# Performance work log

Measured on AMD Instinct MI355X. Metric: run time of the kernel, lower is better.

The kernel has to match this reference:

```python
import jax, jax.numpy as jnp
import numpy as np

N, E, F_IN, H, C = 20000, 320000, 256, 4, 64
D = H * C  # hidden_dim = 256
NEG_SLOPE = 0.2
LN_EPS = 1e-5


def setup_inputs() -> dict:
    key = jax.random.key(0)
    ks = jax.random.split(key, 12)
    x = jax.random.normal(ks[0], (N, F_IN), dtype=jnp.float32)
    # edges guaranteed self-loop-free (PyG GATConv removes then re-adds self loops)
    dst = jax.random.randint(ks[1], (E,), 0, N)
    off = jax.random.randint(ks[2], (E,), 1, N)
    src = (dst + off) % N
    edge_index = jnp.stack([src, dst]).astype(jnp.int64)

    def lin(k, fan_in, shape):
        return jax.random.normal(k, shape, dtype=jnp.float32) / np.sqrt(fan_in)

    W1 = lin(ks[3], F_IN, (F_IN, D)); b1 = jnp.zeros((D,), jnp.float32)
    a_src1 = lin(ks[4], C, (H, C)); a_dst1 = lin(ks[5], C, (H, C))
    W2 = lin(ks[6], D, (D, D)); b2 = jnp.zeros((D,), jnp.float32)
    a_src2 = lin(ks[7], C, (H, C)); a_dst2 = lin(ks[8], C, (H, C))
    g1 = jnp.ones((D,), jnp.float32); be1 = jnp.zeros((D,), jnp.float32)
    g2 = jnp.ones((D,), jnp.float32); be2 = jnp.zeros((D,), jnp.float32)
    attn_w = lin(ks[9], D, (D, 1)); attn_b = jnp.zeros((1,), jnp.float32)
    return dict(x=x, edge_index=edge_index, W1=W1, b1=b1, a_src1=a_src1,
                a_dst1=a_dst1, W2=W2, b2=b2, a_src2=a_src2, a_dst2=a_dst2,
                g1=g1, be1=be1, g2=g2, be2=be2, attn_w=attn_w, attn_b=attn_b)


def _gat_conv(x, src, dst, W, b, a_src, a_dst):
    # x: [N, F] -> h: [N, H, C]
    h = (x @ W).reshape(N, H, C)
    alpha_s = jnp.einsum('nhc,hc->nh', h, a_src)  # [N, H]
    alpha_d = jnp.einsum('nhc,hc->nh', h, a_dst)
    e = jax.nn.leaky_relu(alpha_s[src] + alpha_d[dst], NEG_SLOPE)  # [E', H]
    # segment softmax over edges sharing a destination
    m = jax.ops.segment_max(e, dst, num_segments=N)
    w = jnp.exp(e - m[dst])
    z = jax.ops.segment_sum(w, dst, num_segments=N)
    alpha = w / (z[dst] + 1e-16)
    out = jax.ops.segment_sum(h[src] * alpha[:, :, None], dst, num_segments=N)
    return out.reshape(N, D) + b


def _layernorm(x, g, b):
    mu = x.mean(-1, keepdims=True)
    var = ((x - mu) ** 2).mean(-1, keepdims=True)
    return (x - mu) * jax.lax.rsqrt(var + LN_EPS) * g + b


def reference(x, edge_index, W1, b1, a_src1, a_dst1, W2, b2, a_src2, a_dst2,
              g1, be1, g2, be2, attn_w, attn_b):
    loops = jnp.arange(N, dtype=edge_index.dtype)
    src = jnp.concatenate([edge_index[0], loops])
    dst = jnp.concatenate([edge_index[1], loops])
    x1 = _gat_conv(x, src, dst, W1, b1, a_src1, a_dst1)
    x1 = jax.nn.elu(_layernorm(x1, g1, be1))
    x2 = _gat_conv(x1, src, dst, W2, b2, a_src2, a_dst2)
    x2 = jax.nn.elu(_layernorm(x2, g2, be2) + x1)
    attn = jax.nn.softmax(x2 @ attn_w + attn_b, axis=0)  # softmax over nodes
    pooled = (x2 * attn).sum(axis=0)  # [D]
    return pooled
```

## Files before the change

### kernel.cpp

```cpp
#include <hip/hip_runtime.h>
#include <math.h>

#define N_NODES 20000
#define E_EDGES 320000
#define TOT_E   (E_EDGES + N_NODES)
#define DHID    256
#define NHEAD   4
#define SCAN_NB ((N_NODES + 255) / 256)

typedef float f32x4 __attribute__((ext_vector_type(4)));
typedef short short8 __attribute__((ext_vector_type(8)));
typedef unsigned short ushort;

__device__ __forceinline__ float wave_sum(float v) {
#pragma unroll
  for (int off = 32; off; off >>= 1) v += __shfl_xor(v, off);
  return v;
}
__device__ __forceinline__ ushort f2bf(float f) {
  unsigned u = __float_as_uint(f);
  u += 0x7fffu + ((u >> 16) & 1u);
  return (ushort)(u >> 16);
}
__device__ __forceinline__ float bflo(unsigned u) {
  return __uint_as_float(u << 16);
}
__device__ __forceinline__ float bfhi(unsigned u) {
  return __uint_as_float(u & 0xffff0000u);
}

__global__ void hist_kernel(const int* __restrict__ ei, int* __restrict__ deg) {
  int e = blockIdx.x * blockDim.x + threadIdx.x;
  if (e >= TOT_E) return;
  int dst = (e < E_EDGES) ? ei[E_EDGES + e] : (e - E_EDGES);
  atomicAdd(&deg[dst], 1);
}

__global__ __launch_bounds__(256)
void scan_blocks_kernel(const int* __restrict__ deg, int* __restrict__ bsum) {
  __shared__ int ws[4];
  const int t = threadIdx.x;
  const int i = blockIdx.x * 256 + t;
  int v = (i < N_NODES) ? deg[i] : 0;
  int s = v;
#pragma unroll
  for (int off = 32; off; off >>= 1) s += __shfl_xor(s, off);
  if ((t & 63) == 0) ws[t >> 6] = s;
  __syncthreads();
  if (t == 0) bsum[blockIdx.x] = ws[0] + ws[1] + ws[2] + ws[3];
}

__global__ __launch_bounds__(128)
void scan_tops_kernel(const int* __restrict__ bsum, int* __restrict__ boff) {
  __shared__ int tmp[SCAN_NB];
  const int t = threadIdx.x;
  if (t < SCAN_NB) tmp[t] = bsum[t];
  __syncthreads();
  if (t == 0) {
    int run = 0;
    for (int i = 0; i < SCAN_NB; ++i) { int x = tmp[i]; tmp[i] = run; run += x; }
  }
  __syncthreads();
  if (t < SCAN_NB) boff[t] = tmp[t];
}

__global__ __launch_bounds__(256)
void scan_apply_kernel(const int* __restrict__ deg, const int* __restrict__ boff,
                       int* __restrict__ rowp, int* __restrict__ cur) {
  __shared__ int ws[4];
  const int t = threadIdx.x;
  const int lane = t & 63, w = t >> 6;
  const int i = blockIdx.x * 256 + t;
  int v = (i < N_NODES) ? deg[i] : 0;
  int inc = v;
#pragma unroll
  for (int off = 1; off < 64; off <<= 1) {
    int u = __shfl_up(inc, off);
    if (lane >= off) inc += u;
  }
  if (lane == 63) ws[w] = inc;
  __syncthreads();
  int add = boff[blockIdx.x];
#pragma unroll
  for (int k = 0; k < 4; ++k)
    if (k < w) add += ws[k];
  int exc = add + inc - v;
  if (i < N_NODES) {
    rowp[i] = exc;
    cur[i] = exc;
    if (i == N_NODES - 1) rowp[N_NODES] = exc + v;
  }
}

__global__ void scatter_kernel(const int* __restrict__ ei, int* __restrict__ cur,
                               int* __restrict__ colb) {
  int e = blockIdx.x * blockDim.x + threadIdx.x;
  if (e >= TOT_E) return;
  int src, dst;
  if (e < E_EDGES) { src = ei[e]; dst = ei[E_EDGES + e]; }
  else             { src = dst = e - E_EDGES; }
  int pos = atomicAdd(&cur[dst], 1);
  colb[pos] = src;
}

__global__ __launch_bounds__(256)
void conv_inputs_kernel(const float* __restrict__ W1, const float* __restrict__ W2,
                        const float* __restrict__ x, ushort* __restrict__ Wt1,
                        ushort* __restrict__ Wt2, ushort* __restrict__ xb) {
  const int b = blockIdx.x;
  if (b < 512) {
    const float* W = (b < 256) ? W1 : W2;
    ushort* Wt = (b < 256) ? Wt1 : Wt2;
    const int n = b & 255;
    const int k = threadIdx.x;
    Wt[n * 256 + k] = f2bf(W[k * 256 + n]);
  } else {
    int idx = (b - 512) * 256 + threadIdx.x;
    size_t base = (size_t)idx * 8;
    float4 a = *reinterpret_cast<const float4*>(x + base);
    float4 c = *reinterpret_cast<const float4*>(x + base + 4);
    short8 o;
    o[0] = f2bf(a.x); o[1] = f2bf(a.y); o[2] = f2bf(a.z); o[3] = f2bf(a.w);
    o[4] = f2bf(c.x); o[5] = f2bf(c.y); o[6] = f2bf(c.z); o[7] = f2bf(c.w);
    *reinterpret_cast<short8*>(xb + base) = o;
  }
}

__global__ __launch_bounds__(256)
void gemm_alpha_kernel(const ushort* __restrict__ Ab, const ushort* __restrict__ Wt,
                       const float* __restrict__ asrc, const float* __restrict__ adst,
                       ushort* __restrict__ hout, float* __restrict__ as_,
                       float* __restrict__ ad_) {
  __shared__ ushort hs[32 * 256];

  const int t = threadIdx.x;
  const int w = t >> 6;
  const int l = t & 63;
  const int row0 = blockIdx.x * 32;

  const ushort* abase = Ab + (size_t)(row0 + (l & 15)) * 256 + ((l >> 4) * 8);
  const ushort* bbase = Wt + (size_t)(w * 64 + (l & 15)) * 256 + ((l >> 4) * 8);

  f32x4 acc[2][4];
#pragma unroll
  for (int i = 0; i < 2; ++i)
#pragma unroll
    for (int j = 0; j < 4; ++j) acc[i][j] = (f32x4){0.f, 0.f, 0.f, 0.f};

  short8 a0 = *reinterpret_cast<const short8*>(abase);
  short8 a1 = *reinterpret_cast<const short8*>(abase + 16 * 256);
  short8 b0 = *reinterpret_cast<const short8*>(bbase);
  short8 b1 = *reinterpret_cast<const short8*>(bbase + 16 * 256);
  short8 b2 = *reinterpret_cast<const short8*>(bbase + 32 * 256);
  short8 b3 = *reinterpret_cast<const short8*>(bbase + 48 * 256);
#pragma unroll
  for (int kk = 0; kk < 256; kk += 32) {
    short8 na0, na1, nb0, nb1, nb2, nb3;
    if (kk + 32 < 256) {
      na0 = *reinterpret_cast<const short8*>(abase + kk + 32);
      na1 = *reinterpret_cast<const short8*>(abase + 16 * 256 + kk + 32);
      nb0 = *reinterpret_cast<const short8*>(bbase + kk + 32);
      nb1 = *reinterpret_cast<const short8*>(bbase + 16 * 256 + kk + 32);
      nb2 = *reinterpret_cast<const short8*>(bbase + 32 * 256 + kk + 32);
      nb3 = *reinterpret_cast<const short8*>(bbase + 48 * 256 + kk + 32);
    }
    acc[0][0] = __builtin_amdgcn_mfma_f32_16x16x32_bf16(a0, b0, acc[0][0], 0, 0, 0);
    acc[0][1] = __builtin_amdgcn_mfma_f32_16x16x32_bf16(a0, b1, acc[0][1], 0, 0, 0);
    acc[0][2] = __builtin_amdgcn_mfma_f32_16x16x32_bf16(a0, b2, acc[0][2], 0, 0, 0);
    acc[0][3] = __builtin_amdgcn_mfma_f32_16x16x32_bf16(a0, b3, acc[0][3], 0, 0, 0);
    acc[1][0] = __builtin_amdgcn_mfma_f32_16x16x32_bf16(a1, b0, acc[1][0], 0, 0, 0);
    acc[1][1] = __builtin_amdgcn_mfma_f32_16x16x32_bf16(a1, b1, acc[1][1], 0, 0, 0);
    acc[1][2] = __builtin_amdgcn_mfma_f32_16x16x32_bf16(a1, b2, acc[1][2], 0, 0, 0);
    acc[1][3] = __builtin_amdgcn_mfma_f32_16x16x32_bf16(a1, b3, acc[1][3], 0, 0, 0);
    if (kk + 32 < 256) {
      a0 = na0; a1 = na1; b0 = nb0; b1 = nb1; b2 = nb2; b3 = nb3;
    }
  }

  float asj[4], adj[4];
#pragma unroll
  for (int j = 0; j < 4; ++j) {
    asj[j] = asrc[w * 64 + j * 16 + (l & 15)];
    adj[j] = adst[w * 64 + j * 16 + (l & 15)];
  }
#pragma unroll
  for (int i = 0; i < 2; ++i) {
#pragma unroll
    for (int q = 0; q < 4; ++q) {
      float ps = 0.f, pd = 0.f;
#pragma unroll
      for (int j = 0; j < 4; ++j) {
        ps += acc[i][j][q] * asj[j];
        pd += acc[i][j][q] * adj[j];
      }
#pragma unroll
      for (int off = 1; off < 16; off <<= 1) {
        ps += __shfl_xor(ps, off);
        pd += __shfl_xor(pd, off);
      }
      int row = row0 + i * 16 + (l >> 4) * 4 + q;
      if ((l & 15) == 0) {
        as_[row * 4 + w] = ps;
        ad_[row * 4 + w] = pd;
      }
    }
  }

#pragma unroll
  for (int i = 0; i < 2; ++i)
#pragma unroll
    for (int j = 0; j < 4; ++j)
#pragma unroll
      for (int q = 0; q < 4; ++q) {
        int row = i * 16 + (l >> 4) * 4 + q;
        int col = w * 64 + j * 16 + (l & 15);
        hs[row * 256 + col] = f2bf(acc[i][j][q]);
      }
  __syncthreads();
#pragma unroll
  for (int g = 0; g < 4; ++g) {
    int gi = g * 256 + t;
    int row = gi >> 5;
    int slot = gi & 31;
    *reinterpret_cast<short8*>(hout + (size_t)(row0 + row) * 256 + slot * 8) =
        *reinterpret_cast<const short8*>(&hs[row * 256 + slot * 8]);
  }
}

__global__ __launch_bounds__(256)
void attn_w_kernel(const float* __restrict__ as_, const float* __restrict__ ad_,
                   const int* __restrict__ rowp, const int* __restrict__ colb,
                   float* __restrict__ wbuf, float* __restrict__ zinv) {
  const int t = threadIdx.x;
  const int d = blockIdx.x * 4 + (t >> 6);
  const int l = t & 63;
  const int e16 = l >> 2;
  const int hh = l & 3;
  const int start = rowp[d];
  const int deg = rowp[d + 1] - start;
  const float adv = ad_[d * 4 + hh];

  float M = -INFINITY;
  for (int base = 0; base < deg; base += 16) {
    int i = base + e16;
    float ev = -INFINITY;
    if (i < deg) {
      int s = colb[start + i];
      float e = as_[s * 4 + hh] + adv;
      ev = (e >= 0.f) ? e : 0.2f * e;
    }
    M = fmaxf(M, ev);
  }
#pragma unroll
  for (int off = 4; off < 64; off <<= 1) M = fmaxf(M, __shfl_xor(M, off));

  float z = 0.f;
  for (int base = 0; base < deg; base += 16) {
    int i = base + e16;
    if (i < deg) {
      int s = colb[start + i];
      float e = as_[s * 4 + hh] + adv;
      e = (e >= 0.f) ? e : 0.2f * e;
      float wv = __expf(e - M);
      wbuf[(size_t)(start + i) * 4 + hh] = wv;
      z += wv;
    }
  }
#pragma unroll
  for (int off = 4; off < 64; off <<= 1) z += __shfl_xor(z, off);
  if (e16 == 0) zinv[d * 4 + hh] = 1.f / (z + 1e-16f);
}

__global__ __launch_bounds__(256)
void gather_ln_kernel(const ushort* __restrict__ h, const int* __restrict__ rowp,
                      const int* __restrict__ colb, const float* __restrict__ wbuf,
                      const float* __restrict__ zinv, const float* __restrict__ bias,
                      const float* __restrict__ gamma, const float* __restrict__ beta,
                      const ushort* __restrict__ residb, float* __restrict__ outf,
                      ushort* __restrict__ outb, const float* __restrict__ aw,
                      const float* __restrict__ ab, float* __restrict__ score) {
  const int t = threadIdx.x;
  const int d = blockIdx.x * 4 + (t >> 6);
  const int l = t & 63;
  const int hh = l >> 4;
  const int c0 = l * 4;
  const int start = rowp[d];
  const int deg = rowp[d + 1] - start;

  float a0 = 0.f, a1 = 0.f, a2 = 0.f, a3 = 0.f;
  const ushort* hrow = h + c0;
#pragma unroll 2
  for (int i = 0; i < deg; ++i) {
    const int slot = start + i;
    int s = colb[slot];
    float wv = wbuf[(size_t)slot * 4 + hh];
    uint2 hv = *reinterpret_cast<const uint2*>(hrow + (size_t)s * 256);
    a0 += wv * bflo(hv.x);
    a1 += wv * bfhi(hv.x);
    a2 += wv * bflo(hv.y);
    a3 += wv * bfhi(hv.y);
  }
  const float zi = zinv[d * 4 + hh];
  float4 bi = *reinterpret_cast<const float4*>(bias + c0);
  float v0 = a0 * zi + bi.x, v1 = a1 * zi + bi.y;
  float v2 = a2 * zi + bi.z, v3 = a3 * zi + bi.w;

  float s1 = wave_sum(v0 + v1 + v2 + v3);
  float s2 = wave_sum(v0 * v0 + v1 * v1 + v2 * v2 + v3 * v3);
  float mu = s1 * (1.f / 256.f);
  float var = s2 * (1.f / 256.f) - mu * mu;
  float rstd = rsqrtf(var + 1e-5f);
  float4 ga = *reinterpret_cast<const float4*>(gamma + c0);
  float4 be = *reinterpret_cast<const float4*>(beta + c0);
  float y0 = (v0 - mu) * rstd * ga.x + be.x;
  float y1 = (v1 - mu) * rstd * ga.y + be.y;
  float y2 = (v2 - mu) * rstd * ga.z + be.z;
  float y3 = (v3 - mu) * rstd * ga.w + be.w;
  if (residb) {
    uint2 rv = *reinterpret_cast<const uint2*>(residb + (size_t)d * 256 + c0);
    y0 += bflo(rv.x); y1 += bfhi(rv.x); y2 += bflo(rv.y); y3 += bfhi(rv.y);
  }
  y0 = (y0 > 0.f) ? y0 : expm1f(y0);
  y1 = (y1 > 0.f) ? y1 : expm1f(y1);
  y2 = (y2 > 0.f) ? y2 : expm1f(y2);
  y3 = (y3 > 0.f) ? y3 : expm1f(y3);

  if (outb) {
    uint2 o;
    o.x = ((unsigned)f2bf(y0)) | (((unsigned)f2bf(y1)) << 16);
    o.y = ((unsigned)f2bf(y2)) | (((unsigned)f2bf(y3)) << 16);
    *reinterpret_cast<uint2*>(outb + (size_t)d * 256 + c0) = o;
  }
  if (outf) {
    *reinterpret_cast<float4*>(outf + (size_t)d * 256 + c0) =
        make_float4(y0, y1, y2, y3);
  }
  if (score) {
    float4 aww = *reinterpret_cast<const float4*>(aw + c0);
    float sp = wave_sum(y0 * aww.x + y1 * aww.y + y2 * aww.z + y3 * aww.w);
    if (l == 0) score[d] = sp + ab[0];
  }
}

__global__ __launch_bounds__(256)
void softmax_reduce_kernel(const float* __restrict__ s, float* __restrict__ mz) {
  __shared__ float red[4];
  const int t = threadIdx.x, lane = t & 63, wid = t >> 6;
  float m = -INFINITY;
  for (int n4 = t; n4 < N_NODES / 4; n4 += 256) {
    float4 v = *reinterpret_cast<const float4*>(s + n4 * 4);
    m = fmaxf(m, fmaxf(fmaxf(v.x, v.y), fmaxf(v.z, v.w)));
  }
#pragma unroll
  for (int off = 32; off; off >>= 1) m = fmaxf(m, __shfl_xor(m, off));
  if (lane == 0) red[wid] = m;
  __syncthreads();
  m = fmaxf(fmaxf(red[0], red[1]), fmaxf(red[2], red[3]));
  __syncthreads();
  float z = 0.f;
  for (int n4 = t; n4 < N_NODES / 4; n4 += 256) {
    float4 v = *reinterpret_cast<const float4*>(s + n4 * 4);
    z += __expf(v.x - m) + __expf(v.y - m) + __expf(v.z - m) + __expf(v.w - m);
  }
  z = wave_sum(z);
  if (lane == 0) red[wid] = z;
  __syncthreads();
  if (t == 0) { mz[0] = m; mz[1] = red[0] + red[1] + red[2] + red[3]; }
}

__global__ __launch_bounds__(256)
void pool_partial_kernel(const float* __restrict__ x2, const float* __restrict__ s,
                         const float* __restrict__ mz, float* __restrict__ part) {
  __shared__ float red4[4][256];
  const int t = threadIdx.x, b = blockIdx.x;
  const int c4 = t & 63, rsub = t >> 6;
  const float m = mz[0];
  const float invz = 1.f / mz[1];
  f32x4 acc = (f32x4){0.f, 0.f, 0.f, 0.f};
  for (int n = b * 4 + rsub; n < N_NODES; n += 1024) {
    float w = __expf(s[n] - m);
    float4 xv = *reinterpret_cast<const float4*>(&x2[(size_t)n * 256 + c4 * 4]);
    acc[0] += w * xv.x; acc[1] += w * xv.y; acc[2] += w * xv.z; acc[3] += w * xv.w;
  }
#pragma unroll
  for (int k = 0; k < 4; ++k) red4[rsub][c4 * 4 + k] = acc[k];
  __syncthreads();
  if (t < 256) {
    float v = red4[0][t] + red4[1][t] + red4[2][t] + red4[3][t];
    part[b * 256 + t] = v * invz;
  }
}

__global__ __launch_bounds__(256)
void pool_final_kernel(const float* __restrict__ part, float* __restrict__ out) {
  const int t = threadIdx.x;
  float acc = 0.f;
  for (int b = 0; b < 256; ++b) acc += part[b * 256 + t];
  out[t] = acc;
}

extern "C" void kernel_launch(void* const* d_in, const int* in_sizes, int n_in,
                              void* d_out, int out_size, void* d_ws, size_t ws_size,
                              hipStream_t stream) {
  const float* x      = (const float*)d_in[0];
  const int*   ei     = (const int*)d_in[1];
  const float* W1     = (const float*)d_in[2];
  const float* b1     = (const float*)d_in[3];
  const float* a_src1 = (const float*)d_in[4];
  const float* a_dst1 = (const float*)d_in[5];
  const float* W2     = (const float*)d_in[6];
  const float* b2     = (const float*)d_in[7];
  const float* a_src2 = (const float*)d_in[8];
  const float* a_dst2 = (const float*)d_in[9];
  const float* g1     = (const float*)d_in[10];
  const float* be1    = (const float*)d_in[11];
  const float* g2     = (const float*)d_in[12];
  const float* be2    = (const float*)d_in[13];
  const float* attn_w = (const float*)d_in[14];
  const float* attn_b = (const float*)d_in[15];
  float* out = (float*)d_out;

  char* p = (char*)d_ws;
  auto alloc = [&](size_t bytes) {
    char* r = p;
    p += (bytes + 255) & ~size_t(255);
    return r;
  };
  ushort* h   = (ushort*)alloc((size_t)N_NODES * 256 * 2);
  ushort* xb  = (ushort*)alloc((size_t)N_NODES * 256 * 2);
  ushort* xb1 = (ushort*)alloc((size_t)N_NODES * 256 * 2);
  float* x2   = (float*)alloc((size_t)N_NODES * 256 * 4);
  float* as_  = (float*)alloc((size_t)N_NODES * 4 * 4);
  float* ad_  = (float*)alloc((size_t)N_NODES * 4 * 4);
  float* zinv = (float*)alloc((size_t)N_NODES * 4 * 4);
  float* wbuf = (float*)alloc((size_t)TOT_E * 4 * 4);
  float* sbuf = (float*)alloc((size_t)N_NODES * 4);
  float* mz   = (float*)alloc(256);
  float* part = (float*)alloc((size_t)256 * 256 * 4);
  ushort* wt1 = (ushort*)alloc((size_t)256 * 256 * 2);
  ushort* wt2 = (ushort*)alloc((size_t)256 * 256 * 2);
  int* deg    = (int*)alloc((size_t)N_NODES * 4);
  int* rowp   = (int*)alloc((size_t)(N_NODES + 1) * 4);
  int* cur    = (int*)alloc((size_t)N_NODES * 4);
  int* colb   = (int*)alloc((size_t)TOT_E * 4);
  int* bsum   = (int*)alloc((size_t)SCAN_NB * 4);
  int* boff   = (int*)alloc((size_t)SCAN_NB * 4);

  const int EB = (TOT_E + 255) / 256;
  const int GB = N_NODES / 32;
  const int DB = N_NODES / 4;

  hipMemsetAsync(deg, 0, (size_t)N_NODES * 4, stream);
  hist_kernel<<<EB, 256, 0, stream>>>(ei, deg);
  conv_inputs_kernel<<<512 + N_NODES * 256 / 8 / 256, 256, 0, stream>>>(
      W1, W2, x, wt1, wt2, xb);
  scan_blocks_kernel<<<SCAN_NB, 256, 0, stream>>>(deg, bsum);
  scan_tops_kernel<<<1, 128, 0, stream>>>(bsum, boff);
  scan_apply_kernel<<<SCAN_NB, 256, 0, stream>>>(deg, boff, rowp, cur);
  scatter_kernel<<<EB, 256, 0, stream>>>(ei, cur, colb);

  gemm_alpha_kernel<<<GB, 256, 0, stream>>>(xb, wt1, a_src1, a_dst1, h, as_, ad_);
  attn_w_kernel<<<DB, 256, 0, stream>>>(as_, ad_, rowp, colb, wbuf, zinv);
  gather_ln_kernel<<<DB, 256, 0, stream>>>(h, rowp, colb, wbuf, zinv, b1, g1, be1,
                                           nullptr, nullptr, xb1,
                                           nullptr, nullptr, nullptr);
  gemm_alpha_kernel<<<GB, 256, 0, stream>>>(xb1, wt2, a_src2, a_dst2, h, as_, ad_);
  attn_w_kernel<<<DB, 256, 0, stream>>>(as_, ad_, rowp, colb, wbuf, zinv);
  gather_ln_kernel<<<DB, 256, 0, stream>>>(h, rowp, colb, wbuf, zinv, b2, g2, be2,
                                           xb1, x2, nullptr,
                                           attn_w, attn_b, sbuf);
  softmax_reduce_kernel<<<1, 256, 0, stream>>>(sbuf, mz);
  pool_partial_kernel<<<256, 256, 0, stream>>>(x2, sbuf, mz, part);
  pool_final_kernel<<<1, 256, 0, stream>>>(part, out);
}
```

Baseline: 214.6 us.

## Fuse attention weights into gather-LN kernel, store x2 as bf16, parallelize score softmax

Merges the attention-weight kernel into the gather/LayerNorm kernel. The max is still computed per destination, but exp weights and their sum are recomputed inside the feature gather loop. This removes the wbuf/zinv write and re-read round trip and one launch per layer. The final layer output is stored in bf16 instead of fp32, which halves pooling reads at some precision cost. The single-block score softmax reduction is split into 32 partial blocks plus a combine kernel, and the deg memset is folded into the conversion kernel. The trade-off is an extra as_ gather and exp per edge for every lane of the gather loop.

```diff
diff --git a/kernel.cpp b/kernel.cpp
--- a/kernel.cpp
+++ b/kernel.cpp
@@ -7,6 +7,7 @@
 #define DHID    256
 #define NHEAD   4
 #define SCAN_NB ((N_NODES + 255) / 256)
+#define SPART   32
 
 typedef float f32x4 __attribute__((ext_vector_type(4)));
 typedef short short8 __attribute__((ext_vector_type(8)));
@@ -106,7 +107,8 @@
 __global__ __launch_bounds__(256)
 void conv_inputs_kernel(const float* __restrict__ W1, const float* __restrict__ W2,
                         const float* __restrict__ x, ushort* __restrict__ Wt1,
-                        ushort* __restrict__ Wt2, ushort* __restrict__ xb) {
+                        ushort* __restrict__ Wt2, ushort* __restrict__ xb,
+                        int* __restrict__ deg) {
   const int b = blockIdx.x;
   if (b < 512) {
     const float* W = (b < 256) ? W1 : W2;
@@ -114,7 +116,7 @@
     const int n = b & 255;
     const int k = threadIdx.x;
     Wt[n * 256 + k] = f2bf(W[k * 256 + n]);
-  } else {
+  } else if (b < 512 + N_NODES * 256 / 8 / 256) {
     int idx = (b - 512) * 256 + threadIdx.x;
     size_t base = (size_t)idx * 8;
     float4 a = *reinterpret_cast<const float4*>(x + base);
@@ -123,6 +125,9 @@
     o[0] = f2bf(a.x); o[1] = f2bf(a.y); o[2] = f2bf(a.z); o[3] = f2bf(a.w);
     o[4] = f2bf(c.x); o[5] = f2bf(c.y); o[6] = f2bf(c.z); o[7] = f2bf(c.w);
     *reinterpret_cast<short8*>(xb + base) = o;
+  } else {
+    int idx = (b - (512 + N_NODES * 256 / 8 / 256)) * 256 + threadIdx.x;
+    if (idx < N_NODES) deg[idx] = 0;
   }
 }
 
@@ -228,79 +233,52 @@
 }
 
 __global__ __launch_bounds__(256)
-void attn_w_kernel(const float* __restrict__ as_, const float* __restrict__ ad_,
-                   const int* __restrict__ rowp, const int* __restrict__ colb,
-                   float* __restrict__ wbuf, float* __restrict__ zinv) {
+void attn_gather_ln_kernel(const ushort* __restrict__ h, const float* __restrict__ as_,
+                           const float* __restrict__ ad_, const int* __restrict__ rowp,
+                           const int* __restrict__ colb, const float* __restrict__ bias,
+                           const float* __restrict__ gamma, const float* __restrict__ beta,
+                           const ushort* __restrict__ residb, ushort* __restrict__ outb,
+                           const float* __restrict__ aw, const float* __restrict__ ab,
+                           float* __restrict__ score) {
   const int t = threadIdx.x;
   const int d = blockIdx.x * 4 + (t >> 6);
   const int l = t & 63;
-  const int e16 = l >> 2;
-  const int hh = l & 3;
   const int start = rowp[d];
   const int deg = rowp[d + 1] - start;
+
+  const int e16 = l >> 2, hh = l & 3;
   const float adv = ad_[d * 4 + hh];
-
   float M = -INFINITY;
-  for (int base = 0; base < deg; base += 16) {
-    int i = base + e16;
-    float ev = -INFINITY;
-    if (i < deg) {
-      int s = colb[start + i];
-      float e = as_[s * 4 + hh] + adv;
-      ev = (e >= 0.f) ? e : 0.2f * e;
-    }
-    M = fmaxf(M, ev);
+  for (int i = e16; i < deg; i += 16) {
+    int s = colb[start + i];
+    float e = as_[s * 4 + hh] + adv;
+    e = (e >= 0.f) ? e : 0.2f * e;
+    M = fmaxf(M, e);
   }
 #pragma unroll
   for (int off = 4; off < 64; off <<= 1) M = fmaxf(M, __shfl_xor(M, off));
 
-  float z = 0.f;
-  for (int base = 0; base < deg; base += 16) {
-    int i = base + e16;
-    if (i < deg) {
-      int s = colb[start + i];
-      float e = as_[s * 4 + hh] + adv;
-      e = (e >= 0.f) ? e : 0.2f * e;
-      float wv = __expf(e - M);
-      wbuf[(size_t)(start + i) * 4 + hh] = wv;
-      z += wv;
-    }
-  }
-#pragma unroll
-  for (int off = 4; off < 64; off <<= 1) z += __shfl_xor(z, off);
-  if (e16 == 0) zinv[d * 4 + hh] = 1.f / (z + 1e-16f);
-}
-
-__global__ __launch_bounds__(256)
-void gather_ln_kernel(const ushort* __restrict__ h, const int* __restrict__ rowp,
-                      const int* __restrict__ colb, const float* __restrict__ wbuf,
-                      const float* __restrict__ zinv, const float* __restrict__ bias,
-                      const float* __restrict__ gamma, const float* __restrict__ beta,
-                      const ushort* __restrict__ residb, float* __restrict__ outf,
-                      ushort* __restrict__ outb, const float* __restrict__ aw,
-                      const float* __restrict__ ab, float* __restrict__ score) {
-  const int t = threadIdx.x;
-  const int d = blockIdx.x * 4 + (t >> 6);
-  const int l = t & 63;
-  const int hh = l >> 4;
+  const int gh = l >> 4;
+  const float Mg = __shfl(M, gh);
+  const float adg = __shfl(adv, gh);
+
+  float a0 = 0.f, a1 = 0.f, a2 = 0.f, a3 = 0.f, z = 0.f;
   const int c0 = l * 4;
-  const int start = rowp[d];
-  const int deg = rowp[d + 1] - start;
-
-  float a0 = 0.f, a1 = 0.f, a2 = 0.f, a3 = 0.f;
   const ushort* hrow = h + c0;
 #pragma unroll 2
   for (int i = 0; i < deg; ++i) {
-    const int slot = start + i;
-    int s = colb[slot];
-    float wv = wbuf[(size_t)slot * 4 + hh];
+    int s = colb[start + i];
+    float e = as_[s * 4 + gh] + adg;
+    e = (e >= 0.f) ? e : 0.2f * e;
+    float wv = __expf(e - Mg);
+    z += wv;
     uint2 hv = *reinterpret_cast<const uint2*>(hrow + (size_t)s * 256);
     a0 += wv * bflo(hv.x);
     a1 += wv * bfhi(hv.x);
     a2 += wv * bflo(hv.y);
     a3 += wv * bfhi(hv.y);
   }
-  const float zi = zinv[d * 4 + hh];
+  const float zi = 1.f / (z + 1e-16f);
   float4 bi = *reinterpret_cast<const float4*>(bias + c0);
   float v0 = a0 * zi + bi.x, v1 = a1 * zi + bi.y;
   float v2 = a2 * zi + bi.z, v3 = a3 * zi + bi.w;
@@ -325,16 +303,11 @@
   y2 = (y2 > 0.f) ? y2 : expm1f(y2);
   y3 = (y3 > 0.f) ? y3 : expm1f(y3);
 
-  if (outb) {
-    uint2 o;
-    o.x = ((unsigned)f2bf(y0)) | (((unsigned)f2bf(y1)) << 16);
-    o.y = ((unsigned)f2bf(y2)) | (((unsigned)f2bf(y3)) << 16);
-    *reinterpret_cast<uint2*>(outb + (size_t)d * 256 + c0) = o;
-  }
-  if (outf) {
-    *reinterpret_cast<float4*>(outf + (size_t)d * 256 + c0) =
-        make_float4(y0, y1, y2, y3);
-  }
+  uint2 o;
+  o.x = ((unsigned)f2bf(y0)) | (((unsigned)f2bf(y1)) << 16);
+  o.y = ((unsigned)f2bf(y2)) | (((unsigned)f2bf(y3)) << 16);
+  *reinterpret_cast<uint2*>(outb + (size_t)d * 256 + c0) = o;
+
   if (score) {
     float4 aww = *reinterpret_cast<const float4*>(aw + c0);
     float sp = wave_sum(y0 * aww.x + y1 * aww.y + y2 * aww.z + y3 * aww.w);
@@ -343,14 +316,13 @@
 }
 
 __global__ __launch_bounds__(256)
-void softmax_reduce_kernel(const float* __restrict__ s, float* __restrict__ mz) {
+void score_part_kernel(const float* __restrict__ s, float* __restrict__ pm,
+                       float* __restrict__ pz) {
   __shared__ float red[4];
-  const int t = threadIdx.x, lane = t & 63, wid = t >> 6;
+  const int t = threadIdx.x, b = blockIdx.x;
+  const int lane = t & 63, wid = t >> 6;
   float m = -INFINITY;
-  for (int n4 = t; n4 < N_NODES / 4; n4 += 256) {
-    float4 v = *reinterpret_cast<const float4*>(s + n4 * 4);
-    m = fmaxf(m, fmaxf(fmaxf(v.x, v.y), fmaxf(v.z, v.w)));
-  }
+  for (int n = b * 256 + t; n < N_NODES; n += SPART * 256) m = fmaxf(m, s[n]);
 #pragma unroll
   for (int off = 32; off; off >>= 1) m = fmaxf(m, __shfl_xor(m, off));
   if (lane == 0) red[wid] = m;
@@ -358,18 +330,27 @@
   m = fmaxf(fmaxf(red[0], red[1]), fmaxf(red[2], red[3]));
   __syncthreads();
   float z = 0.f;
-  for (int n4 = t; n4 < N_NODES / 4; n4 += 256) {
-    float4 v = *reinterpret_cast<const float4*>(s + n4 * 4);
-    z += __expf(v.x - m) + __expf(v.y - m) + __expf(v.z - m) + __expf(v.w - m);
-  }
+  for (int n = b * 256 + t; n < N_NODES; n += SPART * 256) z += __expf(s[n] - m);
   z = wave_sum(z);
   if (lane == 0) red[wid] = z;
   __syncthreads();
-  if (t == 0) { mz[0] = m; mz[1] = red[0] + red[1] + red[2] + red[3]; }
-}
-
-__global__ __launch_bounds__(256)
-void pool_partial_kernel(const float* __restrict__ x2, const float* __restrict__ s,
+  if (t == 0) { pm[b] = m; pz[b] = red[0] + red[1] + red[2] + red[3]; }
+}
+
+__global__ __launch_bounds__(64)
+void score_comb_kernel(const float* __restrict__ pm, const float* __restrict__ pz,
+                       float* __restrict__ mz) {
+  const int l = threadIdx.x;
+  float m = (l < SPART) ? pm[l] : -INFINITY;
+#pragma unroll
+  for (int off = 32; off; off >>= 1) m = fmaxf(m, __shfl_xor(m, off));
+  float z = (l < SPART) ? pz[l] * __expf(pm[l] - m) : 0.f;
+  z = wave_sum(z);
+  if (l == 0) { mz[0] = m; mz[1] = z; }
+}
+
+__global__ __launch_bounds__(256)
+void pool_partial_kernel(const ushort* __restrict__ hb2, const float* __restrict__ s,
                          const float* __restrict__ mz, float* __restrict__ part) {
   __shared__ float red4[4][256];
   const int t = threadIdx.x, b = blockIdx.x;
@@ -379,8 +360,11 @@
   f32x4 acc = (f32x4){0.f, 0.f, 0.f, 0.f};
   for (int n = b * 4 + rsub; n < N_NODES; n += 1024) {
     float w = __expf(s[n] - m);
-    float4 xv = *reinterpret_cast<const float4*>(&x2[(size_t)n * 256 + c4 * 4]);
-    acc[0] += w * xv.x; acc[1] += w * xv.y; acc[2] += w * xv.z; acc[3] += w * xv.w;
+    uint2 hv = *reinterpret_cast<const uint2*>(hb2 + (size_t)n * 256 + c4 * 4);
+    acc[0] += w * bflo(hv.x);
+    acc[1] += w * bfhi(hv.x);
+    acc[2] += w * bflo(hv.y);
+    acc[3] += w * bfhi(hv.y);
   }
 #pragma unroll
   for (int k = 0; k < 4; ++k) red4[rsub][c4 * 4 + k] = acc[k];
@@ -429,13 +413,13 @@
   ushort* h   = (ushort*)alloc((size_t)N_NODES * 256 * 2);
   ushort* xb  = (ushort*)alloc((size_t)N_NODES * 256 * 2);
   ushort* xb1 = (ushort*)alloc((size_t)N_NODES * 256 * 2);
-  float* x2   = (float*)alloc((size_t)N_NODES * 256 * 4);
+  ushort* hb2 = (ushort*)alloc((size_t)N_NODES * 256 * 2);
   float* as_  = (float*)alloc((size_t)N_NODES * 4 * 4);
   float* ad_  = (float*)alloc((size_t)N_NODES * 4 * 4);
-  float* zinv = (float*)alloc((size_t)N_NODES * 4 * 4);
-  float* wbuf = (float*)alloc((size_t)TOT_E * 4 * 4);
   float* sbuf = (float*)alloc((size_t)N_NODES * 4);
   float* mz   = (float*)alloc(256);
+  float* pm   = (float*)alloc((size_t)SPART * 4);
+  float* pz   = (float*)alloc((size_t)SPART * 4);
   float* part = (float*)alloc((size_t)256 * 256 * 4);
   ushort* wt1 = (ushort*)alloc((size_t)256 * 256 * 2);
   ushort* wt2 = (ushort*)alloc((size_t)256 * 256 * 2);
@@ -449,27 +433,24 @@
   const int EB = (TOT_E + 255) / 256;
   const int GB = N_NODES / 32;
   const int DB = N_NODES / 4;
-
-  hipMemsetAsync(deg, 0, (size_t)N_NODES * 4, stream);
+  const int XB = N_NODES * 256 / 8 / 256;
+  const int CONVB = 512 + XB + SCAN_NB;
+
+  conv_inputs_kernel<<<CONVB, 256, 0, stream>>>(W1, W2, x, wt1, wt2, xb, deg);
   hist_kernel<<<EB, 256, 0, stream>>>(ei, deg);
-  conv_inputs_kernel<<<512 + N_NODES * 256 / 8 / 256, 256, 0, stream>>>(
-      W1, W2, x, wt1, wt2, xb);
   scan_blocks_kernel<<<SCAN_NB, 256, 0, stream>>>(deg, bsum);
   scan_tops_kernel<<<1, 128, 0, stream>>>(bsum, boff);
   scan_apply_kernel<<<SCAN_NB, 256, 0, stream>>>(deg, boff, rowp, cur);
   scatter_kernel<<<EB, 256, 0, stream>>>(ei, cur, colb);
 
   gemm_alpha_kernel<<<GB, 256, 0, stream>>>(xb, wt1, a_src1, a_dst1, h, as_, ad_);
-  attn_w_kernel<<<DB, 256, 0, stream>>>(as_, ad_, rowp, colb, wbuf, zinv);
-  gather_ln_kernel<<<DB, 256, 0, stream>>>(h, rowp, colb, wbuf, zinv, b1, g1, be1,
-                                           nullptr, nullptr, xb1,
-                                           nullptr, nullptr, nullptr);
+  attn_gather_ln_kernel<<<DB, 256, 0, stream>>>(h, as_, ad_, rowp, colb, b1, g1, be1,
+                                                nullptr, xb1, nullptr, nullptr, nullptr);
   gemm_alpha_kernel<<<GB, 256, 0, stream>>>(xb1, wt2, a_src2, a_dst2, h, as_, ad_);
-  attn_w_kernel<<<DB, 256, 0, stream>>>(as_, ad_, rowp, colb, wbuf, zinv);
-  gather_ln_kernel<<<DB, 256, 0, stream>>>(h, rowp, colb, wbuf, zinv, b2, g2, be2,
-                                           xb1, x2, nullptr,
-                                           attn_w, attn_b, sbuf);
-  softmax_reduce_kernel<<<1, 256, 0, stream>>>(sbuf, mz);
-  pool_partial_kernel<<<256, 256, 0, stream>>>(x2, sbuf, mz, part);
+  attn_gather_ln_kernel<<<DB, 256, 0, stream>>>(h, as_, ad_, rowp, colb, b2, g2, be2,
+                                                xb1, hb2, attn_w, attn_b, sbuf);
+  score_part_kernel<<<SPART, 256, 0, stream>>>(sbuf, pm, pz);
+  score_comb_kernel<<<1, 64, 0, stream>>>(pm, pz, mz);
+  pool_partial_kernel<<<256, 256, 0, stream>>>(hb2, sbuf, mz, part);
   pool_final_kernel<<<1, 256, 0, stream>>>(part, out);
 }
```

Result: faster. 194.0 us (-9.6%).
